# Kernel tuning notes

Hardware: AMD Instinct MI355X
Metric: run time of the kernel (lower is better)

Reference implementation:

```python
import jax, jax.numpy as jnp
import numpy as np

H = 1024
B = 64
S = 1024
V = 50257
L = 3  # GRU layers


def setup_inputs() -> dict:
    key = jax.random.key(0)
    ks = jax.random.split(key, 12)
    sc = 0.02
    return {
        "input_seq": jax.random.randint(ks[0], (B,), 0, V),
        "last_hidden": jax.random.normal(ks[1], (L, B, H), jnp.float32) * sc,
        "encoder_outputs": jax.random.normal(ks[2], (S, B, H), jnp.float32) * sc,
        "emb_table": jax.random.normal(ks[3], (V, H), jnp.float32) * sc,
        "w_ih": jax.random.normal(ks[4], (L, 3 * H, H), jnp.float32) * sc,
        "w_hh": jax.random.normal(ks[5], (L, 3 * H, H), jnp.float32) * sc,
        "b_ih": jax.random.normal(ks[6], (L, 3 * H), jnp.float32) * sc,
        "b_hh": jax.random.normal(ks[7], (L, 3 * H), jnp.float32) * sc,
        "concat_w": jax.random.normal(ks[8], (H, 2 * H), jnp.float32) * sc,
        "concat_b": jax.random.normal(ks[9], (H,), jnp.float32) * sc,
        "out_w": jax.random.normal(ks[10], (V, H), jnp.float32) * sc,
        "out_b": jax.random.normal(ks[11], (V,), jnp.float32) * sc,
    }


def _gru_step(x, h, w_ih, w_hh, b_ih, b_hh):
    # x, h: [B, H]; weights per PyTorch GRU layout (r, z, n gates stacked)
    gi = x @ w_ih.T + b_ih  # [B, 3H]
    gh = h @ w_hh.T + b_hh  # [B, 3H]
    i_r, i_z, i_n = jnp.split(gi, 3, axis=-1)
    h_r, h_z, h_n = jnp.split(gh, 3, axis=-1)
    r = jax.nn.sigmoid(i_r + h_r)
    z = jax.nn.sigmoid(i_z + h_z)
    n = jnp.tanh(i_n + r * h_n)
    return (1.0 - z) * n + z * h


def reference(input_seq, last_hidden, encoder_outputs, emb_table,
              w_ih, w_hh, b_ih, b_hh, concat_w, concat_b, out_w, out_b):
    # Embed current token (decoder uses its own embedding of size hidden_dim).
    x = emb_table[input_seq]  # [B, H]; dropout is identity at eval time
    # 3-layer GRU, single time step.
    new_h = []
    for l in range(L):
        h_l = _gru_step(x, last_hidden[l], w_ih[l], w_hh[l], b_ih[l], b_hh[l])
        new_h.append(h_l)
        x = h_l  # inter-layer dropout is identity at eval time
    hidden = jnp.stack(new_h, axis=0)  # [L, B, H]
    rnn_output = x  # [B, H] (top layer output, seq len 1)
    # Dot attention: score(b, s) = <rnn_output[b], encoder_outputs[s, b]>
    scores = jnp.einsum('bh,sbh->bs', rnn_output, encoder_outputs)  # [B, S]
    attn = jax.nn.softmax(scores, axis=-1)  # [B, S]
    attn_weights = attn[:, None, :]  # [B, 1, S]
    context = jnp.einsum('bs,sbh->bh', attn, encoder_outputs)  # [B, H]
    concat_input = jnp.concatenate([rnn_output, context], axis=-1)  # [B, 2H]
    concat_output = jnp.tanh(concat_input @ concat_w.T + concat_b)  # [B, H]
    output = concat_output @ out_w.T + out_b  # [B, V]
    return (output, hidden, attn_weights)
```

## Files before the change

### kernel.cpp

```cpp
#include <hip/hip_runtime.h>
#include <hip/hip_bf16.h>
#include <float.h>

#define B_ 64
#define H_ 1024
#define S_ 1024
#define V_ 50257
#define VPAD 50304
#define L_ 3
#define G3H 3072
#define N_GATES 6144
#define KSPL_GRU 8
#define KSPL_CAT 16

typedef __attribute__((ext_vector_type(8))) short short8v;
typedef __attribute__((ext_vector_type(4))) float f32x4;

__device__ __forceinline__ ushort rnd_bf16(float x) {
    uint u = __float_as_uint(x);
    return (ushort)((u + 0x7fffu + ((u >> 16) & 1u)) >> 16);
}

__device__ __forceinline__ void split_bf16(float x, ushort& hi, ushort& lo) {
    uint u = __float_as_uint(x);
    uint h = u & 0xffff0000u;
    hi = (ushort)(h >> 16);
    float r = x - __uint_as_float(h);
    uint ur = __float_as_uint(r);
    lo = (ushort)((ur + 0x7fffu + ((ur >> 16) & 1u)) >> 16);
}

__global__ __launch_bounds__(256) void gemm_bf16_lds(
    const float* __restrict__ A0, const int* __restrict__ seq,
    const float* __restrict__ A1, int lda,
    const float* __restrict__ W0, const float* __restrict__ W1, int ldw,
    int Nhalf, float* __restrict__ Cpart, int N, int K) {
    __shared__ ushort AhL[2][64 * 64];
    __shared__ ushort AlL[2][64 * 64];
    __shared__ ushort WtL[2][64 * 64];

    int tid = threadIdx.x;
    int w = tid >> 6, l = tid & 63;
    int lr = l & 15;
    int lk = l >> 4;

    int n0 = blockIdx.x * 64;
    const float* A = A0;
    const float* W = W0;
    const int* sq = seq;
    int ncol0 = n0;
    if (n0 >= Nhalf) { A = A1; W = W1; ncol0 = n0 - Nhalf; sq = nullptr; }

    int srow = tid >> 2;
    int sqk = tid & 3;
    const float* Asrc = A + (size_t)(sq ? sq[srow] : srow) * lda;
    const float* Wsrc = W + (size_t)(ncol0 + srow) * ldw;

    int kChunk = K / gridDim.y;
    int kBeg = blockIdx.y * kChunk;
    int nt = kChunk >> 6;

    union SV { short8v v; ushort u[8]; };

    float4 rA[4], rW[4];
    auto load_regs = [&](int kt) {
        int kb = kBeg + kt * 64 + sqk * 16;
#pragma unroll
        for (int i = 0; i < 4; i++) {
            rA[i] = *(const float4*)&Asrc[kb + i * 4];
            rW[i] = *(const float4*)&Wsrc[kb + i * 4];
        }
    };
    auto write_lds = [&](int buf) {
        int s0 = (2 * sqk) ^ (srow & 7);
        int s1 = (2 * sqk + 1) ^ (srow & 7);
        int base = srow * 64;
        SV h0, h1, l0, l1, q0, q1;
        const float* fa = (const float*)&rA[0];
        const float* fw = (const float*)&rW[0];
#pragma unroll
        for (int j = 0; j < 8; j++) {
            split_bf16(fa[j], h0.u[j], l0.u[j]);
            split_bf16(fa[8 + j], h1.u[j], l1.u[j]);
            q0.u[j] = rnd_bf16(fw[j]);
            q1.u[j] = rnd_bf16(fw[8 + j]);
        }
        *(short8v*)&AhL[buf][base + s0 * 8] = h0.v;
        *(short8v*)&AhL[buf][base + s1 * 8] = h1.v;
        *(short8v*)&AlL[buf][base + s0 * 8] = l0.v;
        *(short8v*)&AlL[buf][base + s1 * 8] = l1.v;
        *(short8v*)&WtL[buf][base + s0 * 8] = q0.v;
        *(short8v*)&WtL[buf][base + s1 * 8] = q1.v;
    };

    f32x4 acc[4];
#pragma unroll
    for (int mt = 0; mt < 4; mt++) acc[mt] = (f32x4){0.f, 0.f, 0.f, 0.f};

    load_regs(0);
    write_lds(0);
    __syncthreads();

    int wrow = w * 16 + lr;
    for (int kt = 0; kt < nt; kt++) {
        if (kt + 1 < nt) load_regs(kt + 1);

        int cur = kt & 1;
#pragma unroll
        for (int ks = 0; ks < 2; ks++) {
            int slot = ks * 4 + lk;
            short8v wf = *(const short8v*)&WtL[cur][wrow * 64 + ((slot ^ (wrow & 7)) << 3)];
#pragma unroll
            for (int mt = 0; mt < 4; mt++) {
                int arow = mt * 16 + lr;
                int so = (slot ^ (arow & 7)) << 3;
                short8v ah = *(const short8v*)&AhL[cur][arow * 64 + so];
                short8v al = *(const short8v*)&AlL[cur][arow * 64 + so];
                acc[mt] = __builtin_amdgcn_mfma_f32_16x16x32_bf16(ah, wf, acc[mt], 0, 0, 0);
                acc[mt] = __builtin_amdgcn_mfma_f32_16x16x32_bf16(al, wf, acc[mt], 0, 0, 0);
            }
        }

        if (kt + 1 < nt) {
            write_lds((kt + 1) & 1);
            __syncthreads();
        }
    }

    float* Pp = Cpart + (size_t)blockIdx.y * 64 * N;
    int col = n0 + wrow;
#pragma unroll
    for (int mt = 0; mt < 4; mt++) {
#pragma unroll
        for (int r = 0; r < 4; r++) {
            int row = mt * 16 + lk * 4 + r;
            Pp[(size_t)row * N + col] = acc[mt][r];
        }
    }
}

__global__ __launch_bounds__(256) void gru_combine_k(
    const float* __restrict__ P, const float* __restrict__ b_ih,
    const float* __restrict__ b_hh, const float* __restrict__ hprev,
    float* __restrict__ hout) {
    int idx = blockIdx.x * 256 + threadIdx.x;
    int b = idx >> 10, j = idx & 1023;
    const size_t stride = (size_t)64 * N_GATES;
    const float* rowp = P + (size_t)b * N_GATES;

    float ir = 0.f, iz = 0.f, in_ = 0.f, hr = 0.f, hz = 0.f, hn = 0.f;
#pragma unroll
    for (int kc = 0; kc < KSPL_GRU; kc++) {
        const float* p = rowp + kc * stride;
        ir += p[j];        iz += p[j + 1024];        in_ += p[j + 2048];
        hr += p[3072 + j]; hz += p[3072 + j + 1024]; hn += p[3072 + j + 2048];
    }
    ir += b_ih[j]; iz += b_ih[j + 1024]; in_ += b_ih[j + 2048];
    hr += b_hh[j]; hz += b_hh[j + 1024]; hn += b_hh[j + 2048];

    float r = 1.f / (1.f + __expf(-(ir + hr)));
    float z = 1.f / (1.f + __expf(-(iz + hz)));
    float n = tanhf(in_ + r * hn);
    float hp = hprev[idx];
    hout[idx] = (1.f - z) * n + z * hp;
}

__global__ __launch_bounds__(256) void attn_pass1(
    const float* __restrict__ rnn, const float* __restrict__ enc,
    float* __restrict__ scores, float* __restrict__ ctxPart,
    float* __restrict__ chunkMax) {
    __shared__ float lm[4];
    __shared__ float lc[4][1024];

    int bid = blockIdx.x;
    int b = bid >> 4, scv = bid & 15;
    int tid = threadIdx.x;
    int w = tid >> 6, lane = tid & 63;

    const float4* rr = (const float4*)(rnn + (size_t)b * H_);
    float4 r0 = rr[0 * 64 + lane], r1 = rr[1 * 64 + lane];
    float4 r2 = rr[2 * 64 + lane], r3 = rr[3 * 64 + lane];

    float m = -FLT_MAX;
    float4 c0 = {0, 0, 0, 0}, c1 = {0, 0, 0, 0}, c2 = {0, 0, 0, 0}, c3 = {0, 0, 0, 0};

    int s0 = scv * 64 + w * 16;
    for (int si = 0; si < 16; si++) {
        int s = s0 + si;
        const float4* er = (const float4*)(enc + ((size_t)s * B_ + b) * H_);
        float4 e0 = er[0 * 64 + lane], e1 = er[1 * 64 + lane];
        float4 e2 = er[2 * 64 + lane], e3 = er[3 * 64 + lane];

        float d = e0.x * r0.x + e0.y * r0.y + e0.z * r0.z + e0.w * r0.w;
        d += e1.x * r1.x + e1.y * r1.y + e1.z * r1.z + e1.w * r1.w;
        d += e2.x * r2.x + e2.y * r2.y + e2.z * r2.z + e2.w * r2.w;
        d += e3.x * r3.x + e3.y * r3.y + e3.z * r3.z + e3.w * r3.w;
#pragma unroll
        for (int off = 32; off; off >>= 1) d += __shfl_xor(d, off, 64);
        if (lane == 0) scores[(size_t)b * S_ + s] = d;

        if (d > m) {
            float scale = __expf(m - d);
            c0.x *= scale; c0.y *= scale; c0.z *= scale; c0.w *= scale;
            c1.x *= scale; c1.y *= scale; c1.z *= scale; c1.w *= scale;
            c2.x *= scale; c2.y *= scale; c2.z *= scale; c2.w *= scale;
            c3.x *= scale; c3.y *= scale; c3.z *= scale; c3.w *= scale;
            m = d;
        }
        float p = __expf(d - m);
        c0.x += p * e0.x; c0.y += p * e0.y; c0.z += p * e0.z; c0.w += p * e0.w;
        c1.x += p * e1.x; c1.y += p * e1.y; c1.z += p * e1.z; c1.w += p * e1.w;
        c2.x += p * e2.x; c2.y += p * e2.y; c2.z += p * e2.z; c2.w += p * e2.w;
        c3.x += p * e3.x; c3.y += p * e3.y; c3.z += p * e3.z; c3.w += p * e3.w;
    }

    if (lane == 0) lm[w] = m;
    __syncthreads();
    float M = fmaxf(fmaxf(lm[0], lm[1]), fmaxf(lm[2], lm[3]));
    float sw = __expf(m - M);
    float4* lw = (float4*)&lc[w][0];
    float4 t;
    t.x = c0.x * sw; t.y = c0.y * sw; t.z = c0.z * sw; t.w = c0.w * sw; lw[0 * 64 + lane] = t;
    t.x = c1.x * sw; t.y = c1.y * sw; t.z = c1.z * sw; t.w = c1.w * sw; lw[1 * 64 + lane] = t;
    t.x = c2.x * sw; t.y = c2.y * sw; t.z = c2.z * sw; t.w = c2.w * sw; lw[2 * 64 + lane] = t;
    t.x = c3.x * sw; t.y = c3.y * sw; t.z = c3.z * sw; t.w = c3.w * sw; lw[3 * 64 + lane] = t;
    __syncthreads();

    float4 s4 = *(const float4*)&lc[0][tid * 4];
    float4 a1 = *(const float4*)&lc[1][tid * 4];
    float4 a2 = *(const float4*)&lc[2][tid * 4];
    float4 a3 = *(const float4*)&lc[3][tid * 4];
    s4.x += a1.x + a2.x + a3.x; s4.y += a1.y + a2.y + a3.y;
    s4.z += a1.z + a2.z + a3.z; s4.w += a1.w + a2.w + a3.w;
    *(float4*)&ctxPart[(size_t)bid * H_ + tid * 4] = s4;
    if (tid == 0) chunkMax[bid] = M;
}

__global__ __launch_bounds__(256) void attn_pass2(
    const float* __restrict__ scores, const float* __restrict__ chunkMax,
    const float* __restrict__ ctxPart, const float* __restrict__ rnn,
    float* __restrict__ attn, float* __restrict__ concat_in) {
    __shared__ float red[256];
    int b = blockIdx.x, tid = threadIdx.x;

    float v[4];
#pragma unroll
    for (int q = 0; q < 4; q++) v[q] = scores[(size_t)b * S_ + q * 256 + tid];
    float mx = fmaxf(fmaxf(v[0], v[1]), fmaxf(v[2], v[3]));
    red[tid] = mx; __syncthreads();
    for (int s = 128; s; s >>= 1) {
        if (tid < s) red[tid] = fmaxf(red[tid], red[tid + s]);
        __syncthreads();
    }
    float M = red[0]; __syncthreads();
    float e[4], sum = 0.f;
#pragma unroll
    for (int q = 0; q < 4; q++) { e[q] = __expf(v[q] - M); sum += e[q]; }
    red[tid] = sum; __syncthreads();
    for (int s = 128; s; s >>= 1) {
        if (tid < s) red[tid] += red[tid + s];
        __syncthreads();
    }
    float inv = 1.f / red[0];
#pragma unroll
    for (int q = 0; q < 4; q++) attn[(size_t)b * S_ + q * 256 + tid] = e[q] * inv;

    float4 acc = {0, 0, 0, 0};
#pragma unroll
    for (int c = 0; c < 16; c++) {
        float scl = __expf(chunkMax[b * 16 + c] - M);
        float4 part = *(const float4*)&ctxPart[((size_t)b * 16 + c) * H_ + tid * 4];
        acc.x += scl * part.x; acc.y += scl * part.y;
        acc.z += scl * part.z; acc.w += scl * part.w;
    }
    acc.x *= inv; acc.y *= inv; acc.z *= inv; acc.w *= inv;
    *(float4*)&concat_in[(size_t)b * 2048 + 1024 + tid * 4] = acc;
    *(float4*)&concat_in[(size_t)b * 2048 + tid * 4] =
        *(const float4*)&rnn[(size_t)b * H_ + tid * 4];
}

__global__ __launch_bounds__(256) void concat_combine_k(const float* __restrict__ P,
                                                        const float* __restrict__ bias,
                                                        ushort* __restrict__ Ahi,
                                                        ushort* __restrict__ Alo) {
    int idx = blockIdx.x * 256 + threadIdx.x;
    int b = idx >> 10, h = idx & 1023;
    float s = 0.f;
#pragma unroll
    for (int kc = 0; kc < KSPL_CAT; kc++) s += P[(size_t)kc * 65536 + (size_t)b * H_ + h];
    float v = tanhf(s + bias[h]);
    ushort hi, lo;
    split_bf16(v, hi, lo);
    Ahi[idx] = hi;
    Alo[idx] = lo;
}

__global__ __launch_bounds__(256) void gemm_out_bf16(
    const ushort* __restrict__ Ahi, const ushort* __restrict__ Alo,
    const float* __restrict__ W, const float* __restrict__ bias,
    float* __restrict__ out) {
    __shared__ ushort WtL[2][32 * 64];

    int tid = threadIdx.x;
    int w = tid >> 6, l = tid & 63;
    int lr = l & 15;
    int lk = l >> 4;

    int n0 = blockIdx.x * 32;

    int srow = tid >> 3;
    int sqk = tid & 7;
    int wrg = n0 + srow;
    const float* Wsrc = W + (size_t)(wrg < V_ ? wrg : 0) * H_;

    union SV { short8v v; ushort u[8]; };

    float4 rW0, rW1;
    auto load_wregs = [&](int kt) {
        int kb = kt * 64 + sqk * 8;
        rW0 = *(const float4*)&Wsrc[kb];
        rW1 = *(const float4*)&Wsrc[kb + 4];
    };
    auto write_lds = [&](int buf) {
        int s = sqk ^ (srow & 7);
        SV p;
        const float* f0 = (const float*)&rW0;
        const float* f1 = (const float*)&rW1;
#pragma unroll
        for (int j = 0; j < 4; j++) {
            p.u[j] = rnd_bf16(f0[j]);
            p.u[j + 4] = rnd_bf16(f1[j]);
        }
        *(short8v*)&WtL[buf][srow * 64 + s * 8] = p.v;
    };

    f32x4 acc[2];
    acc[0] = (f32x4){0.f, 0.f, 0.f, 0.f};
    acc[1] = (f32x4){0.f, 0.f, 0.f, 0.f};

    load_wregs(0);
    write_lds(0);
    __syncthreads();

    const ushort* Ah = Ahi + (size_t)(w * 16 + lr) * H_;
    const ushort* Al = Alo + (size_t)(w * 16 + lr) * H_;

    for (int kt = 0; kt < 16; kt++) {
        if (kt + 1 < 16) load_wregs(kt + 1);

        int kb = kt * 64 + lk * 8;
        short8v ah0 = *(const short8v*)&Ah[kb];
        short8v al0 = *(const short8v*)&Al[kb];
        short8v ah1 = *(const short8v*)&Ah[kb + 32];
        short8v al1 = *(const short8v*)&Al[kb + 32];

        int cur = kt & 1;
#pragma unroll
        for (int nt = 0; nt < 2; nt++) {
            int wr = nt * 16 + lr;
            short8v wf0 = *(const short8v*)&WtL[cur][wr * 64 + ((lk ^ (wr & 7)) << 3)];
            short8v wf1 = *(const short8v*)&WtL[cur][wr * 64 + (((4 + lk) ^ (wr & 7)) << 3)];
            acc[nt] = __builtin_amdgcn_mfma_f32_16x16x32_bf16(ah0, wf0, acc[nt], 0, 0, 0);
            acc[nt] = __builtin_amdgcn_mfma_f32_16x16x32_bf16(al0, wf0, acc[nt], 0, 0, 0);
            acc[nt] = __builtin_amdgcn_mfma_f32_16x16x32_bf16(ah1, wf1, acc[nt], 0, 0, 0);
            acc[nt] = __builtin_amdgcn_mfma_f32_16x16x32_bf16(al1, wf1, acc[nt], 0, 0, 0);
        }

        if (kt + 1 < 16) write_lds(cur ^ 1);
        __syncthreads();
    }

    float* et = (float*)&WtL[0][0];
#pragma unroll
    for (int nt = 0; nt < 2; nt++) {
#pragma unroll
        for (int r = 0; r < 4; r++) {
            int row = w * 16 + lk * 4 + r;
            et[row * 32 + nt * 16 + lr] = acc[nt][r];
        }
    }
    __syncthreads();

    int col = tid & 31;
    int rg = tid >> 5;
    int gc = n0 + col;
    if (gc < V_) {
        float b = bias[gc];
#pragma unroll
        for (int rr = 0; rr < 8; rr++) {
            int row = rg * 8 + rr;
            out[(size_t)row * V_ + gc] = et[row * 32 + col] + b;
        }
    }
}

extern "C" void kernel_launch(void* const* d_in, const int* in_sizes, int n_in,
                              void* d_out, int out_size, void* d_ws, size_t ws_size,
                              hipStream_t stream) {
    const int* seq = (const int*)d_in[0];
    const float* last_hidden = (const float*)d_in[1];
    const float* enc = (const float*)d_in[2];
    const float* emb = (const float*)d_in[3];
    const float* w_ih = (const float*)d_in[4];
    const float* w_hh = (const float*)d_in[5];
    const float* b_ih = (const float*)d_in[6];
    const float* b_hh = (const float*)d_in[7];
    const float* concat_w = (const float*)d_in[8];
    const float* concat_b = (const float*)d_in[9];
    const float* out_w = (const float*)d_in[10];
    const float* out_b = (const float*)d_in[11];

    float* out = (float*)d_out;
    float* out_hidden = out + (size_t)B_ * V_;
    float* out_attn = out_hidden + (size_t)L_ * B_ * H_;

    float* ws = (float*)d_ws;
    float* gatesP = ws;
    float* scores = gatesP + 3145728;
    float* chunkMax = scores + 65536;
    float* ctxPart = chunkMax + 1024;
    float* concat_in = ctxPart + 1048576;
    float* concatP = concat_in + 131072;
    ushort* Ahi = (ushort*)(concatP + 1048576);
    ushort* Alo = Ahi + 65536;

    for (int l = 0; l < L_; l++) {
        const float* xl = (l == 0) ? emb : out_hidden + (size_t)(l - 1) * B_ * H_;
        const int* sq = (l == 0) ? seq : nullptr;
        const float* hl = last_hidden + (size_t)l * B_ * H_;
        gemm_bf16_lds<<<dim3(N_GATES / 64, KSPL_GRU), 256, 0, stream>>>(
            xl, sq, hl, H_,
            w_ih + (size_t)l * G3H * H_, w_hh + (size_t)l * G3H * H_, H_, G3H,
            gatesP, N_GATES, H_);
        gru_combine_k<<<256, 256, 0, stream>>>(gatesP, b_ih + (size_t)l * G3H,
                                               b_hh + (size_t)l * G3H, hl,
                                               out_hidden + (size_t)l * B_ * H_);
    }
    const float* rnn = out_hidden + (size_t)2 * B_ * H_;

    attn_pass1<<<1024, 256, 0, stream>>>(rnn, enc, scores, ctxPart, chunkMax);
    attn_pass2<<<64, 256, 0, stream>>>(scores, chunkMax, ctxPart, rnn,
                                       out_attn, concat_in);

    gemm_bf16_lds<<<dim3(H_ / 64, KSPL_CAT), 256, 0, stream>>>(
        concat_in, nullptr, concat_in, 2048, concat_w, concat_w, 2048, 1 << 30,
        concatP, H_, 2048);
    concat_combine_k<<<256, 256, 0, stream>>>(concatP, concat_b, Ahi, Alo);

    gemm_out_bf16<<<VPAD / 32, 256, 0, stream>>>(Ahi, Alo, out_w, out_b, out);
}
```

Baseline: 193.2 us.

## Stage half of W tile per phase in LDS, prefetch A fragments in registers

The output-projection GEMM now loads a 32x512 bf16 tile of W into LDS in two large phases instead of double-buffered 64-wide K steps. This cuts the barriers per block from 16 to about 4 and gives each thread 16 float4 loads in flight at once. Inside each phase the A hi/lo fragments for the next K step are prefetched into registers. In exchange, LDS use grows to 32 KB per block, which may lower occupancy, and global loads no longer overlap with MFMA work across phases.

```diff
diff --git a/kernel.cpp b/kernel.cpp
--- a/kernel.cpp
+++ b/kernel.cpp
@@ -299,7 +299,7 @@
     const ushort* __restrict__ Ahi, const ushort* __restrict__ Alo,
     const float* __restrict__ W, const float* __restrict__ bias,
     float* __restrict__ out) {
-    __shared__ ushort WtL[2][32 * 64];
+    __shared__ ushort WtL[32 * 512];
 
     int tid = threadIdx.x;
     int w = tid >> 6, l = tid & 63;
@@ -309,68 +309,79 @@
     int n0 = blockIdx.x * 32;
 
     int srow = tid >> 3;
-    int sqk = tid & 7;
+    int sc = tid & 7;
     int wrg = n0 + srow;
     const float* Wsrc = W + (size_t)(wrg < V_ ? wrg : 0) * H_;
 
     union SV { short8v v; ushort u[8]; };
-
-    float4 rW0, rW1;
-    auto load_wregs = [&](int kt) {
-        int kb = kt * 64 + sqk * 8;
-        rW0 = *(const float4*)&Wsrc[kb];
-        rW1 = *(const float4*)&Wsrc[kb + 4];
-    };
-    auto write_lds = [&](int buf) {
-        int s = sqk ^ (srow & 7);
-        SV p;
-        const float* f0 = (const float*)&rW0;
-        const float* f1 = (const float*)&rW1;
-#pragma unroll
-        for (int j = 0; j < 4; j++) {
-            p.u[j] = rnd_bf16(f0[j]);
-            p.u[j + 4] = rnd_bf16(f1[j]);
-        }
-        *(short8v*)&WtL[buf][srow * 64 + s * 8] = p.v;
-    };
 
     f32x4 acc[2];
     acc[0] = (f32x4){0.f, 0.f, 0.f, 0.f};
     acc[1] = (f32x4){0.f, 0.f, 0.f, 0.f};
 
-    load_wregs(0);
-    write_lds(0);
-    __syncthreads();
-
     const ushort* Ah = Ahi + (size_t)(w * 16 + lr) * H_;
     const ushort* Al = Alo + (size_t)(w * 16 + lr) * H_;
 
-    for (int kt = 0; kt < 16; kt++) {
-        if (kt + 1 < 16) load_wregs(kt + 1);
-
-        int kb = kt * 64 + lk * 8;
+    for (int ph = 0; ph < 2; ph++) {
+        int kb0 = ph * 512;
+
+        {
+            const float* src = Wsrc + kb0 + sc * 64;
+            int rbase = srow * 512;
+            int r7 = srow & 7;
+#pragma unroll
+            for (int j = 0; j < 8; j++) {
+                float4 f0 = *(const float4*)&src[j * 8];
+                float4 f1 = *(const float4*)&src[j * 8 + 4];
+                SV p;
+                const float* a = (const float*)&f0;
+                const float* b = (const float*)&f1;
+#pragma unroll
+                for (int i = 0; i < 4; i++) {
+                    p.u[i] = rnd_bf16(a[i]);
+                    p.u[i + 4] = rnd_bf16(b[i]);
+                }
+                int slot = sc * 8 + j;
+                *(short8v*)&WtL[rbase + ((slot ^ r7) << 3)] = p.v;
+            }
+        }
+        __syncthreads();
+
+        int kb = kb0 + lk * 8;
         short8v ah0 = *(const short8v*)&Ah[kb];
         short8v al0 = *(const short8v*)&Al[kb];
         short8v ah1 = *(const short8v*)&Ah[kb + 32];
         short8v al1 = *(const short8v*)&Al[kb + 32];
 
-        int cur = kt & 1;
-#pragma unroll
-        for (int nt = 0; nt < 2; nt++) {
-            int wr = nt * 16 + lr;
-            short8v wf0 = *(const short8v*)&WtL[cur][wr * 64 + ((lk ^ (wr & 7)) << 3)];
-            short8v wf1 = *(const short8v*)&WtL[cur][wr * 64 + (((4 + lk) ^ (wr & 7)) << 3)];
-            acc[nt] = __builtin_amdgcn_mfma_f32_16x16x32_bf16(ah0, wf0, acc[nt], 0, 0, 0);
-            acc[nt] = __builtin_amdgcn_mfma_f32_16x16x32_bf16(al0, wf0, acc[nt], 0, 0, 0);
-            acc[nt] = __builtin_amdgcn_mfma_f32_16x16x32_bf16(ah1, wf1, acc[nt], 0, 0, 0);
-            acc[nt] = __builtin_amdgcn_mfma_f32_16x16x32_bf16(al1, wf1, acc[nt], 0, 0, 0);
-        }
-
-        if (kt + 1 < 16) write_lds(cur ^ 1);
+        for (int kt = 0; kt < 8; kt++) {
+            short8v nah0, nal0, nah1, nal1;
+            if (kt + 1 < 8) {
+                int nkb = kb0 + (kt + 1) * 64 + lk * 8;
+                nah0 = *(const short8v*)&Ah[nkb];
+                nal0 = *(const short8v*)&Al[nkb];
+                nah1 = *(const short8v*)&Ah[nkb + 32];
+                nal1 = *(const short8v*)&Al[nkb + 32];
+            }
+
+#pragma unroll
+            for (int nt = 0; nt < 2; nt++) {
+                int wr = nt * 16 + lr;
+                int r7 = wr & 7;
+                int sb = kt * 8;
+                short8v wf0 = *(const short8v*)&WtL[wr * 512 + (((sb + lk) ^ r7) << 3)];
+                short8v wf1 = *(const short8v*)&WtL[wr * 512 + (((sb + 4 + lk) ^ r7) << 3)];
+                acc[nt] = __builtin_amdgcn_mfma_f32_16x16x32_bf16(ah0, wf0, acc[nt], 0, 0, 0);
+                acc[nt] = __builtin_amdgcn_mfma_f32_16x16x32_bf16(al0, wf0, acc[nt], 0, 0, 0);
+                acc[nt] = __builtin_amdgcn_mfma_f32_16x16x32_bf16(ah1, wf1, acc[nt], 0, 0, 0);
+                acc[nt] = __builtin_amdgcn_mfma_f32_16x16x32_bf16(al1, wf1, acc[nt], 0, 0, 0);
+            }
+
+            ah0 = nah0; al0 = nal0; ah1 = nah1; al1 = nal1;
+        }
         __syncthreads();
     }
 
-    float* et = (float*)&WtL[0][0];
+    float* et = (float*)&WtL[0];
 #pragma unroll
     for (int nt = 0; nt < 2; nt++) {
 #pragma unroll
```

Result: slower. 218.9 us (+13.3%).
